# Kernel tuning notes

Hardware: AMD Instinct MI355X
Metric: run time of the kernel (lower is better)

Reference implementation:

```python
import jax, jax.numpy as jnp
import numpy as np

N = 4096
SIGMA = 1.0
TWOPI = 2.0 * np.pi
EPS = 1e-6
SQRT2 = np.sqrt(2.0)
SELF_C = 1.0 / (SIGMA * TWOPI ** 1.5)  # self-interaction constant


def setup_inputs() -> dict:
    key = jax.random.key(0)
    k1, k2 = jax.random.split(key)
    positions = jax.random.normal(k1, (N, 3), dtype=jnp.float32) * 5.0
    q = jax.random.normal(k2, (N, 1), dtype=jnp.float32)
    return {"positions": positions, "q": q}


def reference(positions, q):
    # Real-space Ewald sum (aperiodic cell path of EwaldPotential, exponent=1,
    # remove_self_interaction=False, compute_field=True).
    # positions: [N,3], q: [N,1]
    r_ij = positions[None, :, :] - positions[:, None, :]          # [N,N,3]
    d = jnp.linalg.norm(r_ij, axis=-1)                             # [N,N]
    conv = jax.scipy.special.erf(d / (SIGMA * SQRT2))              # [N,N]
    w = conv / (d + EPS)                                           # fused erf * 1/r weight
    # pot = sum_ij q_i q_j w_ij / (2*pi*2)
    pot = jnp.sum((q @ q.T) * w) / (TWOPI * 2.0)
    # field_j = sum_i q_i w_ij / (2*pi)   (w is symmetric; use w.T for faithfulness)
    field = (w.T @ q) / TWOPI                                      # [N,1]
    # self-interaction term (remove_self_interaction == False, exponent == 1)
    pot = pot + jnp.sum(q ** 2) * SELF_C
    field = field + q * (2.0 * SELF_C)
    # concatenate [pot (1,), field (N,)] -> [N+1]
    return jnp.concatenate([pot.reshape(1), field.reshape(-1)])
```

## Files before the change

### kernel.cpp

```cpp
#include <hip/hip_runtime.h>


#define NPART 4096
#define JBLK 256
#define ICHUNK 64
#define NCHUNK (NPART / ICHUNK)

__device__ __forceinline__ float erf_pos(float x) {
    float t = __builtin_amdgcn_rcpf(fmaf(0.3275911f, x, 1.0f));
    float poly = fmaf(fmaf(fmaf(fmaf(1.061405429f, t, -1.453152027f),
                                t, 1.421413741f),
                           t, -0.284496736f),
                      t, 0.254829592f) * t;
    float e = __expf(-x * x);
    return fmaf(-poly, e, 1.0f);
}

__global__ __launch_bounds__(JBLK) void ewald_pairs(
        const float* __restrict__ pos,
        const float* __restrict__ q,
        float* __restrict__ s) {
    __shared__ float4 sp[ICHUNK];

    const int tid = threadIdx.x;
    const int j = blockIdx.x * JBLK + tid;
    const int i0 = blockIdx.y * ICHUNK;

    if (tid < ICHUNK) {
        const int i = i0 + tid;
        sp[tid] = make_float4(pos[3 * i], pos[3 * i + 1], pos[3 * i + 2], q[i]);
    }

    const float px = pos[3 * j];
    const float py = pos[3 * j + 1];
    const float pz = pos[3 * j + 2];

    __syncthreads();

    float acc = 0.0f;
#pragma unroll 8
    for (int k = 0; k < ICHUNK; ++k) {
        float4 p = sp[k];
        float dx = p.x - px;
        float dy = p.y - py;
        float dz = p.z - pz;
        float d2 = fmaf(dx, dx, fmaf(dy, dy, dz * dz));
        float d = __builtin_amdgcn_sqrtf(d2);
        float x = d * 0.7071067811865475f;
        float erfv = erf_pos(x);
        float w = erfv * __builtin_amdgcn_rcpf(d + 1e-6f);
        w = ((i0 + k) == j) ? 0.0f : w;
        acc = fmaf(p.w, w, acc);
    }

    atomicAdd(&s[j], acc);
}

__global__ __launch_bounds__(1024) void ewald_finalize(
        const float* __restrict__ q,
        const float* __restrict__ s,
        float* __restrict__ out) {
    const float INV2PI = 0.15915494309189535f;
    const float INV4PI = 0.07957747154594767f;
    const float SELFC  = 0.06349363593424097f;

    float pot = 0.0f;
    for (int j = threadIdx.x; j < NPART; j += 1024) {
        float sj = s[j];
        float qj = q[j];
        out[1 + j] = fmaf(sj, INV2PI, qj * (2.0f * SELFC));
        pot = fmaf(qj * sj, INV4PI, pot);
        pot = fmaf(qj * qj, SELFC, pot);
    }

#pragma unroll
    for (int off = 32; off > 0; off >>= 1) pot += __shfl_down(pot, off);

    __shared__ float red[16];
    const int wid = threadIdx.x >> 6;
    if ((threadIdx.x & 63) == 0) red[wid] = pot;
    __syncthreads();
    if (threadIdx.x == 0) {
        float tot = 0.0f;
#pragma unroll
        for (int w = 0; w < 16; ++w) tot += red[w];
        out[0] = tot;
    }
}

extern "C" void kernel_launch(void* const* d_in, const int* in_sizes, int n_in,
                              void* d_out, int out_size, void* d_ws, size_t ws_size,
                              hipStream_t stream) {
    const float* pos = (const float*)d_in[0];
    const float* q   = (const float*)d_in[1];
    float* out = (float*)d_out;
    float* s   = (float*)d_ws;

    hipMemsetAsync(s, 0, NPART * sizeof(float), stream);

    dim3 grid(NPART / JBLK, NCHUNK);
    hipLaunchKernelGGL(ewald_pairs, grid, dim3(JBLK), 0, stream, pos, q, s);
    hipLaunchKernelGGL(ewald_finalize, dim3(1), dim3(1024), 0, stream, q, s, out);
}
```

Measured before the change: 73.85 us.

## Replace atomics and memset with partial buffers; use rsqrt-based erf/r evaluation

The pair kernel now writes per-chunk partial field sums to a workspace buffer and computes per-block potential partials, instead of doing atomicAdd into a memset-cleared array. The finalize kernel is spread over 17 blocks: 16 reduce partials per column and one reduces the potential. The inner loop uses rsq to get d and 1/d, approximates 1/(d+eps) with a first-order correction, and computes exp(-d2/2) directly from d2. This drops the memset launch, atomics and the serial single-block finalize, and trims sqrt/rcp work per pair. In exchange it writes 64x4096 floats of workspace and slightly changes the 1/(d+eps) numerics.

```diff
diff --git a/kernel.cpp b/kernel.cpp
--- a/kernel.cpp
+++ b/kernel.cpp
@@ -5,22 +5,15 @@
 #define JBLK 256
 #define ICHUNK 64
 #define NCHUNK (NPART / ICHUNK)
-
-__device__ __forceinline__ float erf_pos(float x) {
-    float t = __builtin_amdgcn_rcpf(fmaf(0.3275911f, x, 1.0f));
-    float poly = fmaf(fmaf(fmaf(fmaf(1.061405429f, t, -1.453152027f),
-                                t, 1.421413741f),
-                           t, -0.284496736f),
-                      t, 0.254829592f) * t;
-    float e = __expf(-x * x);
-    return fmaf(-poly, e, 1.0f);
-}
+#define NJT (NPART / JBLK)
 
 __global__ __launch_bounds__(JBLK) void ewald_pairs(
         const float* __restrict__ pos,
         const float* __restrict__ q,
-        float* __restrict__ s) {
+        float* __restrict__ partial,
+        float* __restrict__ potblk) {
     __shared__ float4 sp[ICHUNK];
+    __shared__ float red[4];
 
     const int tid = threadIdx.x;
     const int j = blockIdx.x * JBLK + tid;
@@ -34,6 +27,7 @@
     const float px = pos[3 * j];
     const float py = pos[3 * j + 1];
     const float pz = pos[3 * j + 2];
+    const float qj = q[j];
 
     __syncthreads();
 
@@ -45,46 +39,64 @@
         float dy = p.y - py;
         float dz = p.z - pz;
         float d2 = fmaf(dx, dx, fmaf(dy, dy, dz * dz));
-        float d = __builtin_amdgcn_sqrtf(d2);
-        float x = d * 0.7071067811865475f;
-        float erfv = erf_pos(x);
-        float w = erfv * __builtin_amdgcn_rcpf(d + 1e-6f);
+        float r  = __builtin_amdgcn_rsqf(d2);
+        float d  = d2 * r;
+        float inv = r * fmaf(-1e-6f, r, 1.0f);
+        float t  = __builtin_amdgcn_rcpf(fmaf(0.23165390651f, d, 1.0f));
+        float e  = __expf(-0.5f * d2);
+        float poly = fmaf(fmaf(fmaf(fmaf(1.061405429f, t, -1.453152027f),
+                                    t, 1.421413741f),
+                               t, -0.284496736f),
+                          t, 0.254829592f) * t;
+        float w = fmaf(-poly, e, 1.0f) * inv;
         w = ((i0 + k) == j) ? 0.0f : w;
         acc = fmaf(p.w, w, acc);
     }
 
-    atomicAdd(&s[j], acc);
+    partial[blockIdx.y * NPART + j] = acc;
+
+    float pj = qj * acc;
+#pragma unroll
+    for (int off = 32; off > 0; off >>= 1) pj += __shfl_down(pj, off);
+    if ((tid & 63) == 0) red[tid >> 6] = pj;
+    __syncthreads();
+    if (tid == 0)
+        potblk[blockIdx.y * NJT + blockIdx.x] = red[0] + red[1] + red[2] + red[3];
 }
 
-__global__ __launch_bounds__(1024) void ewald_finalize(
+__global__ __launch_bounds__(256) void ewald_finalize(
         const float* __restrict__ q,
-        const float* __restrict__ s,
+        const float* __restrict__ partial,
+        const float* __restrict__ potblk,
         float* __restrict__ out) {
     const float INV2PI = 0.15915494309189535f;
     const float INV4PI = 0.07957747154594767f;
     const float SELFC  = 0.06349363593424097f;
 
-    float pot = 0.0f;
-    for (int j = threadIdx.x; j < NPART; j += 1024) {
-        float sj = s[j];
-        float qj = q[j];
-        out[1 + j] = fmaf(sj, INV2PI, qj * (2.0f * SELFC));
-        pot = fmaf(qj * sj, INV4PI, pot);
-        pot = fmaf(qj * qj, SELFC, pot);
-    }
+    const int tid = threadIdx.x;
 
+    if (blockIdx.x < NJT) {
+        const int j = blockIdx.x * 256 + tid;
+        float s = 0.0f;
+#pragma unroll 8
+        for (int c = 0; c < NCHUNK; ++c) s += partial[c * NPART + j];
+        out[1 + j] = fmaf(s, INV2PI, q[j] * (2.0f * SELFC));
+    } else {
+        float p = 0.0f;
 #pragma unroll
-    for (int off = 32; off > 0; off >>= 1) pot += __shfl_down(pot, off);
-
-    __shared__ float red[16];
-    const int wid = threadIdx.x >> 6;
-    if ((threadIdx.x & 63) == 0) red[wid] = pot;
-    __syncthreads();
-    if (threadIdx.x == 0) {
-        float tot = 0.0f;
+        for (int c = 0; c < 4; ++c) p += potblk[c * 256 + tid];
+        p *= INV4PI;
 #pragma unroll
-        for (int w = 0; w < 16; ++w) tot += red[w];
-        out[0] = tot;
+        for (int k = 0; k < 16; ++k) {
+            float qq = q[tid * 16 + k];
+            p = fmaf(qq * qq, SELFC, p);
+        }
+#pragma unroll
+        for (int off = 32; off > 0; off >>= 1) p += __shfl_down(p, off);
+        __shared__ float red[4];
+        if ((tid & 63) == 0) red[tid >> 6] = p;
+        __syncthreads();
+        if (tid == 0) out[0] = red[0] + red[1] + red[2] + red[3];
     }
 }
 
@@ -94,11 +106,10 @@
     const float* pos = (const float*)d_in[0];
     const float* q   = (const float*)d_in[1];
     float* out = (float*)d_out;
-    float* s   = (float*)d_ws;
-
-    hipMemsetAsync(s, 0, NPART * sizeof(float), stream);
+    float* partial = (float*)d_ws;
+    float* potblk  = partial + NCHUNK * NPART;
 
     dim3 grid(NPART / JBLK, NCHUNK);
-    hipLaunchKernelGGL(ewald_pairs, grid, dim3(JBLK), 0, stream, pos, q, s);
-    hipLaunchKernelGGL(ewald_finalize, dim3(1), dim3(1024), 0, stream, q, s, out);
+    hipLaunchKernelGGL(ewald_pairs, grid, dim3(JBLK), 0, stream, pos, q, partial, potblk);
+    hipLaunchKernelGGL(ewald_finalize, dim3(NJT + 1), dim3(256), 0, stream, q, partial, potblk, out);
 }
```

Result: faster. 72.03 us (-2.5%).
